# Kernel tuning notes

Hardware: AMD Instinct MI355X
Metric: run time of the kernel (lower is better)

## Reference

```python
import jax, jax.numpy as jnp
import numpy as np

E, T, IN, OUT = 8, 16384, 1024, 1024  # n_groups, total_tokens, in_features, out_features


def setup_inputs() -> dict:
    key = jax.random.key(0)
    kx, kw, ks = jax.random.split(key, 3)
    x = jax.random.normal(kx, (T, IN), dtype=jnp.float32)
    # kaiming_uniform-ish scale for weight [E, OUT, IN]
    weight = jax.random.normal(kw, (E, OUT, IN), dtype=jnp.float32) * (1.0 / np.sqrt(IN))
    # ragged segment lengths that sum exactly to T (random cut points)
    cuts = jnp.sort(jax.random.randint(ks, (E - 1,), 0, T + 1)).astype(jnp.int32)
    seg_lens = jnp.diff(
        jnp.concatenate([jnp.zeros((1,), jnp.int32), cuts, jnp.full((1,), T, jnp.int32)])
    )
    return {"x": x, "weight": weight, "seg_lens": seg_lens}


def reference(x, weight, seg_lens):
    # Grouped GEMM: row t of x is multiplied by weight[g(t)].T where g(t) is the
    # segment (expert) that token t falls into per seg_lens. trans_b=True.
    n_groups = weight.shape[0]
    bounds = jnp.cumsum(seg_lens)                                  # [E]
    seg_id = jnp.searchsorted(bounds, jnp.arange(x.shape[0]), side="right")  # [T]
    y = jnp.zeros((x.shape[0], weight.shape[1]), dtype=x.dtype)
    for e in range(n_groups):  # small fixed loop over groups
        y = y + jnp.where((seg_id == e)[:, None], x @ weight[e].T, 0)
    return y
```

## Files before the change

kernel.cpp:

```cpp
#include <hip/hip_runtime.h>

#define T_TOK  16384
#define IN_F   1024
#define OUT_F  1024
#define NE     8
#define BM     128
#define BN     128
#define BK     32
#define NTHREADS 256
#define ROW_TILE_SLOTS 136

typedef __bf16 bf16;
typedef bf16  bf16x4 __attribute__((ext_vector_type(4)));
typedef bf16  bf16x8 __attribute__((ext_vector_type(8)));
typedef float f32x4  __attribute__((ext_vector_type(4)));

__global__ __launch_bounds__(NTHREADS)
void grouped_gemm_f32io_bf16(const float* __restrict__ x,
                             const float* __restrict__ wgt,
                             const int*  __restrict__ seg_lens,
                             float* __restrict__ out)
{
    __shared__ __align__(16) bf16 As[BM * BK];
    __shared__ __align__(16) bf16 Bs[BN * BK];

    const int m    = blockIdx.y;
    const int col0 = blockIdx.x * BN;

    int e_sel = -1, row0 = 0, rows = 0;
    {
        int start = 0, acct = 0;
        #pragma unroll
        for (int e = 0; e < NE; ++e) {
            int len = seg_lens[e];
            int nt  = (len + BM - 1) >> 7;
            if (e_sel < 0 && m >= acct && m < acct + nt) {
                e_sel = e;
                row0  = start + (m - acct) * BM;
                int rem = start + len - row0;
                rows = rem < BM ? rem : BM;
            }
            acct  += nt;
            start += len;
        }
    }
    if (e_sel < 0) return;

    const int tid  = threadIdx.x;
    const int lane = tid & 63;
    const int wave = tid >> 6;
    const int wm   = (wave >> 1) * 64;
    const int wn   = (wave & 1) * 64;
    const int quad = lane >> 4;
    const int l16  = lane & 15;

    const float* wbase = wgt + ((size_t)e_sel * OUT_F + (size_t)col0) * IN_F;

    f32x4 acc[4][4] = {};

    for (int k0 = 0; k0 < IN_F; k0 += BK) {
        f32x4 a_st[4], b_st[4];
        #pragma unroll
        for (int t = 0; t < 4; ++t) {
            int c  = t * NTHREADS + tid;
            int rg = row0 + (c >> 3);
            if (rg > T_TOK - 1) rg = T_TOK - 1;
            a_st[t] = *(const f32x4*)(x + (size_t)rg * IN_F + k0 + (c & 7) * 4);
            b_st[t] = *(const f32x4*)(wbase + (size_t)(c >> 3) * IN_F + k0 + (c & 7) * 4);
        }

        __syncthreads();

        #pragma unroll
        for (int t = 0; t < 4; ++t) {
            int c = t * NTHREADS + tid;
            bf16x4 ha, hb;
            #pragma unroll
            for (int j = 0; j < 4; ++j) { ha[j] = (bf16)a_st[t][j]; hb[j] = (bf16)b_st[t][j]; }
            *(bf16x4*)(&As[(c >> 3) * BK + (c & 7) * 4]) = ha;
            *(bf16x4*)(&Bs[(c >> 3) * BK + (c & 7) * 4]) = hb;
        }
        __syncthreads();

        bf16x8 af[4], bfr[4];
        #pragma unroll
        for (int t = 0; t < 4; ++t)
            af[t] = *(const bf16x8*)(&As[(wm + t * 16 + l16) * BK + quad * 8]);
        #pragma unroll
        for (int u = 0; u < 4; ++u)
            bfr[u] = *(const bf16x8*)(&Bs[(wn + u * 16 + l16) * BK + quad * 8]);

        #pragma unroll
        for (int t = 0; t < 4; ++t)
            #pragma unroll
            for (int u = 0; u < 4; ++u)
                acc[t][u] = __builtin_amdgcn_mfma_f32_16x16x32_bf16(
                    af[t], bfr[u], acc[t][u], 0, 0, 0);
    }

    #pragma unroll
    for (int t = 0; t < 4; ++t) {
        #pragma unroll
        for (int r = 0; r < 4; ++r) {
            int row = wm + t * 16 + quad * 4 + r;
            if (row < rows) {
                size_t ob = (size_t)(row0 + row) * OUT_F + col0;
                #pragma unroll
                for (int u = 0; u < 4; ++u)
                    out[ob + wn + u * 16 + l16] = acc[t][u][r];
            }
        }
    }
}

extern "C" void kernel_launch(void* const* d_in, const int* in_sizes, int n_in,
                              void* d_out, int out_size, void* d_ws, size_t ws_size,
                              hipStream_t stream) {
    const float* x   = (const float*)d_in[0];
    const float* wgt = (const float*)d_in[1];
    const int*   seg = (const int*)d_in[2];
    float* out = (float*)d_out;

    dim3 grid(OUT_F / BN, ROW_TILE_SLOTS, 1);
    dim3 block(NTHREADS, 1, 1);
    grouped_gemm_f32io_bf16<<<grid, block, 0, stream>>>(x, wgt, seg, out);
}
```

Baseline: 214.1 us.

## Pre-convert inputs to bf16 in workspace and load tiles via global_load_lds

Adds a separate conversion kernel that writes bf16 copies of x and the weights into the workspace. A new GEMM kernel then streams bf16 tiles straight into LDS with global_load_lds, instead of loading fp32 into registers and converting per tile. This halves GEMM-side global traffic and drops the register staging and conversion work from the main loop. The cost is an extra full read/write pass over both inputs. The original fused kernel is kept as a fallback when the workspace is too small.

```diff
diff --git a/kernel.cpp b/kernel.cpp
--- a/kernel.cpp
+++ b/kernel.cpp
@@ -15,11 +15,37 @@
 typedef bf16  bf16x8 __attribute__((ext_vector_type(8)));
 typedef float f32x4  __attribute__((ext_vector_type(4)));
 
+#define NX_ELEM ((size_t)T_TOK * IN_F)
+#define NW_ELEM ((size_t)NE * OUT_F * IN_F)
+#define WS_NEED ((NX_ELEM + NW_ELEM) * sizeof(bf16))
+
 __global__ __launch_bounds__(NTHREADS)
-void grouped_gemm_f32io_bf16(const float* __restrict__ x,
-                             const float* __restrict__ wgt,
-                             const int*  __restrict__ seg_lens,
-                             float* __restrict__ out)
+void cvt_to_bf16(const float* __restrict__ x, const float* __restrict__ w,
+                 bf16* __restrict__ xb, bf16* __restrict__ wb)
+{
+    const size_t NX8 = NX_ELEM / 8;
+    const size_t NW8 = NW_ELEM / 8;
+    size_t stride = (size_t)gridDim.x * blockDim.x;
+    for (size_t i = (size_t)blockIdx.x * blockDim.x + threadIdx.x;
+         i < NX8 + NW8; i += stride) {
+        const float* src;
+        bf16* dst;
+        if (i < NX8) { src = x + i * 8;          dst = xb + i * 8; }
+        else         { src = w + (i - NX8) * 8;  dst = wb + (i - NX8) * 8; }
+        f32x4 v0 = *(const f32x4*)(src);
+        f32x4 v1 = *(const f32x4*)(src + 4);
+        bf16x8 h;
+        #pragma unroll
+        for (int j = 0; j < 4; ++j) { h[j] = (bf16)v0[j]; h[4 + j] = (bf16)v1[j]; }
+        *(bf16x8*)dst = h;
+    }
+}
+
+__global__ __launch_bounds__(NTHREADS)
+void grouped_gemm_bf16(const bf16* __restrict__ x,
+                       const bf16* __restrict__ wgt,
+                       const int*  __restrict__ seg_lens,
+                       float* __restrict__ out)
 {
     __shared__ __align__(16) bf16 As[BM * BK];
     __shared__ __align__(16) bf16 Bs[BN * BK];
@@ -54,6 +80,105 @@
     const int quad = lane >> 4;
     const int l16  = lane & 15;
 
+    const bf16* wbase = wgt + ((size_t)e_sel * OUT_F + (size_t)col0) * IN_F;
+
+    f32x4 acc[4][4] = {};
+
+    for (int k0 = 0; k0 < IN_F; k0 += BK) {
+        __syncthreads();
+
+        #pragma unroll
+        for (int t = 0; t < 2; ++t) {
+            int c  = t * NTHREADS + tid;
+            int rg = row0 + (c >> 2);
+            if (rg > T_TOK - 1) rg = T_TOK - 1;
+            const bf16* gp = x + (size_t)rg * IN_F + k0 + (c & 3) * 8;
+            __builtin_amdgcn_global_load_lds(
+                (const __attribute__((address_space(1))) void*)gp,
+                (__attribute__((address_space(3))) void*)(&As[c * 8]),
+                16, 0, 0);
+        }
+        #pragma unroll
+        for (int t = 0; t < 2; ++t) {
+            int c = t * NTHREADS + tid;
+            const bf16* gp = wbase + (size_t)(c >> 2) * IN_F + k0 + (c & 3) * 8;
+            __builtin_amdgcn_global_load_lds(
+                (const __attribute__((address_space(1))) void*)gp,
+                (__attribute__((address_space(3))) void*)(&Bs[c * 8]),
+                16, 0, 0);
+        }
+        __syncthreads();
+
+        bf16x8 af[4], bfr[4];
+        #pragma unroll
+        for (int t = 0; t < 4; ++t)
+            af[t] = *(const bf16x8*)(&As[(wm + t * 16 + l16) * BK + quad * 8]);
+        #pragma unroll
+        for (int u = 0; u < 4; ++u)
+            bfr[u] = *(const bf16x8*)(&Bs[(wn + u * 16 + l16) * BK + quad * 8]);
+
+        #pragma unroll
+        for (int t = 0; t < 4; ++t)
+            #pragma unroll
+            for (int u = 0; u < 4; ++u)
+                acc[t][u] = __builtin_amdgcn_mfma_f32_16x16x32_bf16(
+                    af[t], bfr[u], acc[t][u], 0, 0, 0);
+    }
+
+    #pragma unroll
+    for (int t = 0; t < 4; ++t) {
+        #pragma unroll
+        for (int r = 0; r < 4; ++r) {
+            int row = wm + t * 16 + quad * 4 + r;
+            if (row < rows) {
+                size_t ob = (size_t)(row0 + row) * OUT_F + col0;
+                #pragma unroll
+                for (int u = 0; u < 4; ++u)
+                    out[ob + wn + u * 16 + l16] = acc[t][u][r];
+            }
+        }
+    }
+}
+
+__global__ __launch_bounds__(NTHREADS)
+void grouped_gemm_f32io_fused(const float* __restrict__ x,
+                              const float* __restrict__ wgt,
+                              const int*  __restrict__ seg_lens,
+                              float* __restrict__ out)
+{
+    __shared__ __align__(16) bf16 As[BM * BK];
+    __shared__ __align__(16) bf16 Bs[BN * BK];
+
+    const int m    = blockIdx.y;
+    const int col0 = blockIdx.x * BN;
+
+    int e_sel = -1, row0 = 0, rows = 0;
+    {
+        int start = 0, acct = 0;
+        #pragma unroll
+        for (int e = 0; e < NE; ++e) {
+            int len = seg_lens[e];
+            int nt  = (len + BM - 1) >> 7;
+            if (e_sel < 0 && m >= acct && m < acct + nt) {
+                e_sel = e;
+                row0  = start + (m - acct) * BM;
+                int rem = start + len - row0;
+                rows = rem < BM ? rem : BM;
+            }
+            acct  += nt;
+            start += len;
+        }
+    }
+    if (e_sel < 0) return;
+
+    const int tid  = threadIdx.x;
+    const int lane = tid & 63;
+    const int wave = tid >> 6;
+    const int wm   = (wave >> 1) * 64;
+    const int wn   = (wave & 1) * 64;
+    const int quad = lane >> 4;
+    const int l16  = lane & 15;
+
     const float* wbase = wgt + ((size_t)e_sel * OUT_F + (size_t)col0) * IN_F;
 
     f32x4 acc[4][4] = {};
@@ -68,9 +193,7 @@
             a_st[t] = *(const f32x4*)(x + (size_t)rg * IN_F + k0 + (c & 7) * 4);
             b_st[t] = *(const f32x4*)(wbase + (size_t)(c >> 3) * IN_F + k0 + (c & 7) * 4);
         }
-
-        __syncthreads();
-
+        __syncthreads();
         #pragma unroll
         for (int t = 0; t < 4; ++t) {
             int c = t * NTHREADS + tid;
@@ -121,7 +244,15 @@
     const int*   seg = (const int*)d_in[2];
     float* out = (float*)d_out;
 
-    dim3 grid(OUT_F / BN, ROW_TILE_SLOTS, 1);
     dim3 block(NTHREADS, 1, 1);
-    grouped_gemm_f32io_bf16<<<grid, block, 0, stream>>>(x, wgt, seg, out);
-}
+    dim3 grid2(OUT_F / BN, ROW_TILE_SLOTS, 1);
+
+    if (ws_size >= WS_NEED) {
+        bf16* xb = (bf16*)d_ws;
+        bf16* wb = xb + NX_ELEM;
+        cvt_to_bf16<<<3072, block, 0, stream>>>(x, wgt, xb, wb);
+        grouped_gemm_bf16<<<grid2, block, 0, stream>>>(xb, wb, seg, out);
+    } else {
+        grouped_gemm_f32io_fused<<<grid2, block, 0, stream>>>(x, wgt, seg, out);
+    }
+}
```

Result: no change. 217.5 us (+1.6%).
